# Kernel tuning notes

Hardware: AMD Instinct MI355X
Metric: run time of the kernel (lower is better)

Reference implementation:

```python
import jax, jax.numpy as jnp
import numpy as np

B, S, D, P = 8, 2048, 512, 64  # batch, seq, num_embed_hidden, num_attention_project


def setup_inputs() -> dict:
    key = jax.random.key(0)
    ks = jax.random.split(key, 9)
    sd = 1.0 / np.sqrt(D)
    sp = 1.0 / np.sqrt(P)
    return {
        "query": jax.random.normal(ks[0], (B, S, D), dtype=jnp.float32),
        "attention_mask": jnp.ones((B, S), dtype=jnp.float32),
        "Wq": jax.random.uniform(ks[1], (D, P), jnp.float32, -sd, sd),
        "bq": jax.random.uniform(ks[2], (P,), jnp.float32, -sd, sd),
        "Wk": jax.random.uniform(ks[3], (D, P), jnp.float32, -sd, sd),
        "bk": jax.random.uniform(ks[4], (P,), jnp.float32, -sd, sd),
        "Wv": jax.random.uniform(ks[5], (D, P), jnp.float32, -sd, sd),
        "bv": jax.random.uniform(ks[6], (P,), jnp.float32, -sd, sd),
        "Wo": jax.random.uniform(ks[7], (P, D), jnp.float32, -sp, sp),
        "bo": jax.random.uniform(ks[8], (D,), jnp.float32, -sp, sp),
    }


def reference(query, attention_mask, Wq, bq, Wk, bk, Wv, bv, Wo, bo):
    q = jnp.einsum("bsd,dp->bsp", query, Wq) + bq  # [B,S,P]
    k = jnp.einsum("bsd,dp->bsp", query, Wk) + bk
    v = jnp.einsum("bsd,dp->bsp", query, Wv) + bv
    scores = jnp.einsum("bsp,btp->bst", q, k) / jnp.sqrt(jnp.float32(P))  # [B,S,S]
    # Faithful to original: mask broadcast over last axis via unsqueeze(-1) -> masks rows
    scores = scores + (1.0 - attention_mask[:, :, None]) * -10000.0
    weights = jax.nn.softmax(scores, axis=-1)
    weighted = jnp.einsum("bst,btp->bsp", weights, v)
    return jnp.einsum("bsp,pd->bsd", weighted, Wo) + bo
```

## Files before the change

kernel.cpp:

```cpp
#include <hip/hip_runtime.h>
#include <hip/hip_bf16.h>
#include <math.h>

constexpr int B = 8;
constexpr int S = 2048;
constexpr int D = 512;
constexpr int P = 64;
constexpr float SCALE = 0.125f;

typedef short bf16x8 __attribute__((ext_vector_type(8)));
typedef float f32x4 __attribute__((ext_vector_type(4)));
typedef unsigned int u32;

__device__ __forceinline__ unsigned short f2bf(float x) {
  __hip_bfloat16 h = __float2bfloat16(x);
  return __builtin_bit_cast(unsigned short, h);
}
__device__ __forceinline__ float bf2f(unsigned short u) {
  unsigned int v = (unsigned int)u << 16;
  return __builtin_bit_cast(float, v);
}


__global__ __launch_bounds__(256) void prep_w(
    const float* __restrict__ Wq, const float* __restrict__ Wk,
    const float* __restrict__ Wv, const float* __restrict__ Wo,
    unsigned short* __restrict__ Bfrag, unsigned short* __restrict__ Wofrag) {
  const int i = blockIdx.x * 256 + threadIdx.x;
  if (i < 192 * 512) {
    const int d = i / 192;
    const int n = i - d * 192;
    const float* W = (n < 64) ? Wq : (n < 128) ? Wk : Wv;
    const float val = W[d * 64 + (n & 63)];
    const int nt = n >> 4, l15 = n & 15;
    const int k16 = d >> 5, l4 = (d >> 3) & 3, j = d & 7;
    Bfrag[(((nt * 16 + k16) * 4 + l4) * 16 + l15) * 8 + j] = f2bf(val);
  }
  if (i < 64 * 512) {
    const int k = i >> 9;
    const int n = i & 511;
    const float val = Wo[k * 512 + n];
    const int ct = n >> 4, l15 = n & 15;
    const int h = k >> 5, l4 = (k >> 3) & 3, j = k & 7;
    Wofrag[(((ct * 2 + h) * 4 + l4) * 16 + l15) * 8 + j] = f2bf(val);
  }
}

__global__ __launch_bounds__(256, 4) void qkv_mfma(
    const float* __restrict__ query, const unsigned short* __restrict__ Bfrag,
    const float* __restrict__ bq, const float* __restrict__ bk,
    const float* __restrict__ bv, unsigned short* __restrict__ qfrag,
    unsigned short* __restrict__ kfrag, unsigned short* __restrict__ vfrag) {
  __shared__ __align__(16) unsigned short Aq[16 * 512];

  const int tid = threadIdx.x;
  const int w = tid >> 6;
  const int l = tid & 63;
  const int l15 = l & 15;
  const int l4 = l >> 4;
  const int s0 = blockIdx.x * 16;
  const int kb0 = blockIdx.x & 15;

  const float* qsrc = query + (size_t)s0 * D;
#pragma unroll
  for (int step = 0; step < 4; ++step) {
    const int row = step * 4 + w;
    const float* pf = qsrc + row * D + l * 8;
    const float4 x = *(const float4*)pf;
    const float4 y = *(const float4*)(pf + 4);
    bf16x8 u;
    u[0] = (short)f2bf(x.x); u[1] = (short)f2bf(x.y);
    u[2] = (short)f2bf(x.z); u[3] = (short)f2bf(x.w);
    u[4] = (short)f2bf(y.x); u[5] = (short)f2bf(y.y);
    u[6] = (short)f2bf(y.z); u[7] = (short)f2bf(y.w);
    *(bf16x8*)&Aq[row * 512 + ((l ^ (row & 7)) << 3)] = u;
  }
  __syncthreads();

  f32x4 acc[3];
#pragma unroll
  for (int nt = 0; nt < 3; ++nt) acc[nt] = (f32x4){0.f, 0.f, 0.f, 0.f};

#pragma unroll
  for (int kk = 0; kk < 16; ++kk) {
    const int k16 = (kk + kb0) & 15;
    const int aslot = (k16 * 4 + l4) ^ (l15 & 7);
    const bf16x8 af = *(const bf16x8*)&Aq[l15 * 512 + (aslot << 3)];
#pragma unroll
    for (int nt = 0; nt < 3; ++nt) {
      const int ntg = w * 3 + nt;
      const bf16x8 bf =
          *(const bf16x8*)(Bfrag + ((size_t)(ntg * 16 + k16) * 64 + l) * 8);
      acc[nt] = __builtin_amdgcn_mfma_f32_16x16x32_bf16(af, bf, acc[nt], 0, 0,
                                                        0);
    }
  }

  const int b = s0 >> 11;
  const size_t bbase = (size_t)b * (S * P);
#pragma unroll
  for (int nt = 0; nt < 3; ++nt) {
    const int col = w * 48 + nt * 16 + l15;
    const int mat = col >> 6;
    const int p = col & 63;
    const float bb = ((mat == 0) ? bq : (mat == 1) ? bk : bv)[p];
#pragma unroll
    for (int r = 0; r < 4; ++r) {
      const int s = s0 + l4 * 4 + r;
      const int t = s & 2047;
      const float vl = acc[nt][r] + bb;
      if (mat == 2) {
        const int tb = t >> 5, chv = (t >> 3) & 3, jv = t & 7;
        const int pcv = p >> 4, rowv = p & 15;
        vfrag[bbase + (((size_t)(tb * 4 + pcv) * 4 + chv) * 16 + rowv) * 8 +
              jv] = f2bf(vl);
      } else {
        const int tile = t >> 4, rowin = t & 15;
        const int h = p >> 5, chp = (p >> 3) & 3, j = p & 7;
        unsigned short* dst = (mat == 0) ? qfrag : kfrag;
        dst[bbase + (((size_t)(tile * 2 + h) * 4 + chp) * 16 + rowin) * 8 +
            j] = f2bf(mat == 0 ? vl * SCALE : vl);
      }
    }
  }
}

__global__ __launch_bounds__(1024, 4) void attn_fused(
    const unsigned short* __restrict__ qfrag,
    const unsigned short* __restrict__ kfrag,
    const unsigned short* __restrict__ vfrag,
    const unsigned short* __restrict__ Wofrag, const float* __restrict__ bo,
    float* __restrict__ out) {
  __shared__ __align__(16) unsigned char smem[131072];
  __shared__ float l_s[16][32];

  const int tid = threadIdx.x;
  const int w = tid >> 6;
  const int lane = tid & 63;
  const int l15 = lane & 15;
  const int l4 = lane >> 4;
  const int qg = w & 1;
  const int th = w >> 1;

  const int blk = blockIdx.x;
  const int b = blk & 7;
  const int qt = blk >> 3;
  const int s0 = qt * 64;
  const int wst = qt & 3;

  const size_t bbase = (size_t)b * (S * P);
  const unsigned short* qf = qfrag + bbase;
  const unsigned short* kf = kfrag + bbase;
  const unsigned short* vf = vfrag + bbase;

  unsigned short* e_w = (unsigned short*)smem + w * 4096;

  bf16x8 aq[2][2];
#pragma unroll
  for (int st = 0; st < 2; ++st)
#pragma unroll
    for (int h = 0; h < 2; ++h)
      aq[st][h] =
          *(const bf16x8*)(qf +
                           ((size_t)(((s0 >> 4) + qg * 2 + st) * 2 + h) * 64 +
                            lane) *
                               8);

  f32x4 acc[2][4];
#pragma unroll
  for (int st = 0; st < 2; ++st)
#pragma unroll
    for (int pc = 0; pc < 4; ++pc) acc[st][pc] = (f32x4){0.f, 0.f, 0.f, 0.f};
  float lpart[2][4] = {{0.f, 0.f, 0.f, 0.f}, {0.f, 0.f, 0.f, 0.f}};

  for (int win = 0; win < 4; ++win) {
    const int wi = (win + wst) & 3;
    const int t0 = th * 256 + wi * 64;
    unsigned short* e_s = e_w + (win & 1) * 2048;

    bf16x8 bk[4][2];
#pragma unroll
    for (int nt = 0; nt < 4; ++nt)
#pragma unroll
      for (int h = 0; h < 2; ++h)
        bk[nt][h] =
            *(const bf16x8*)(kf +
                             ((size_t)(((t0 >> 4) + nt) * 2 + h) * 64 + lane) *
                                 8);

#pragma unroll
    for (int st = 0; st < 2; ++st) {
      f32x4 sc[4];
#pragma unroll
      for (int nt = 0; nt < 4; ++nt) {
        f32x4 c = (f32x4){0.f, 0.f, 0.f, 0.f};
        c = __builtin_amdgcn_mfma_f32_16x16x32_bf16(aq[st][0], bk[nt][0], c, 0,
                                                    0, 0);
        sc[nt] = __builtin_amdgcn_mfma_f32_16x16x32_bf16(aq[st][1], bk[nt][1],
                                                         c, 0, 0, 0);
      }
#pragma unroll
      for (int nt = 0; nt < 4; ++nt) {
        const int ch = nt * 2 + (l15 >> 3);
#pragma unroll
        for (int r = 0; r < 4; ++r) {
          const int rr = l4 * 4 + r;
          const unsigned short eu = f2bf(__expf(sc[nt][r]));
          lpart[st][r] += bf2f(eu);
          e_s[st * 1024 + rr * 64 + ((ch ^ (rr & 7)) << 3) + (l15 & 7)] = eu;
        }
      }
    }

    bf16x8 bv[4][2];
#pragma unroll
    for (int pc = 0; pc < 4; ++pc)
#pragma unroll
      for (int kk = 0; kk < 2; ++kk)
        bv[pc][kk] =
            *(const bf16x8*)(vf +
                             ((size_t)(((t0 >> 5) + kk) * 4 + pc) * 64 + lane) *
                                 8);

#pragma unroll
    for (int st = 0; st < 2; ++st) {
      bf16x8 ae[2];
#pragma unroll
      for (int kk = 0; kk < 2; ++kk)
        ae[kk] = *(const bf16x8*)&e_s[st * 1024 + l15 * 64 +
                                      (((kk * 4 + l4) ^ (l15 & 7)) << 3)];
#pragma unroll
      for (int pc = 0; pc < 4; ++pc) {
        acc[st][pc] = __builtin_amdgcn_mfma_f32_16x16x32_bf16(
            ae[0], bv[pc][0], acc[st][pc], 0, 0, 0);
        acc[st][pc] = __builtin_amdgcn_mfma_f32_16x16x32_bf16(
            ae[1], bv[pc][1], acc[st][pc], 0, 0, 0);
      }
    }
  }

#pragma unroll
  for (int st = 0; st < 2; ++st)
#pragma unroll
    for (int r = 0; r < 4; ++r) {
      float v = lpart[st][r];
      v += __shfl_xor(v, 1, 64);
      v += __shfl_xor(v, 2, 64);
      v += __shfl_xor(v, 4, 64);
      v += __shfl_xor(v, 8, 64);
      if (l15 == 0) l_s[w][st * 16 + l4 * 4 + r] = v;
    }

  __syncthreads();

  float* pacc = (float*)smem;
  if (th > 0) {
#pragma unroll
    for (int st = 0; st < 2; ++st)
#pragma unroll
      for (int pc = 0; pc < 4; ++pc)
#pragma unroll
        for (int r = 0; r < 4; ++r)
          pacc[((size_t)(qg * 7 + th - 1) * 32 + st * 16 + l4 * 4 + r) * 64 +
               pc * 16 + l15] = acc[st][pc][r];
  }
  __syncthreads();

  unsigned short* wnorm = (unsigned short*)(smem + 114688);
  if (th == 0) {
#pragma unroll
    for (int st = 0; st < 2; ++st) {
      float rl[4];
#pragma unroll
      for (int r = 0; r < 4; ++r) {
        const int row = st * 16 + l4 * 4 + r;
        float ls = 0.f;
#pragma unroll
        for (int t8 = 0; t8 < 8; ++t8) ls += l_s[t8 * 2 + qg][row];
        rl[r] = 1.f / ls;
      }
#pragma unroll
      for (int pc = 0; pc < 4; ++pc)
#pragma unroll
        for (int r = 0; r < 4; ++r) {
          float s = acc[st][pc][r];
#pragma unroll
          for (int j = 0; j < 7; ++j)
            s += pacc[((size_t)(qg * 7 + j) * 32 + st * 16 + l4 * 4 + r) * 64 +
                      pc * 16 + l15];
          wnorm[(qg * 32 + st * 16 + l4 * 4 + r) * 64 + pc * 16 + l15] =
              f2bf(s * rl[r]);
        }
    }
  }
  __syncthreads();

  const int sub = w & 3;
  const int chq = w >> 2;
  const bf16x8 a0 = *(const bf16x8*)&wnorm[(sub * 16 + l15) * 64 + l4 * 8];
  const bf16x8 a1 =
      *(const bf16x8*)&wnorm[(sub * 16 + l15) * 64 + 32 + l4 * 8];
  const size_t orow0 = (size_t)b * S + s0 + sub * 16;
#pragma unroll
  for (int ct = 0; ct < 8; ++ct) {
    const int ctg = chq * 8 + ((ct + (blk & 7)) & 7);
    const bf16x8 b0 =
        *(const bf16x8*)(Wofrag + ((size_t)(ctg * 2 + 0) * 64 + lane) * 8);
    const bf16x8 b1 =
        *(const bf16x8*)(Wofrag + ((size_t)(ctg * 2 + 1) * 64 + lane) * 8);
    f32x4 c = (f32x4){0.f, 0.f, 0.f, 0.f};
    c = __builtin_amdgcn_mfma_f32_16x16x32_bf16(a0, b0, c, 0, 0, 0);
    c = __builtin_amdgcn_mfma_f32_16x16x32_bf16(a1, b1, c, 0, 0, 0);
    const int col = ctg * 16 + l15;
    const float bb = bo[col];
#pragma unroll
    for (int r = 0; r < 4; ++r)
      out[(orow0 + l4 * 4 + r) * D + col] = c[r] + bb;
  }
}

extern "C" void kernel_launch(void* const* d_in, const int* in_sizes, int n_in,
                              void* d_out, int out_size, void* d_ws,
                              size_t ws_size, hipStream_t stream) {
  const float* query = (const float*)d_in[0];
  const float* Wq = (const float*)d_in[2];
  const float* bq = (const float*)d_in[3];
  const float* Wk = (const float*)d_in[4];
  const float* bk = (const float*)d_in[5];
  const float* Wv = (const float*)d_in[6];
  const float* bv = (const float*)d_in[7];
  const float* Wo = (const float*)d_in[8];
  const float* bo = (const float*)d_in[9];
  float* out = (float*)d_out;

  const size_t proj = (size_t)B * S * P;
  unsigned short* qfr = (unsigned short*)d_ws;
  unsigned short* kfr = qfr + proj;
  unsigned short* vfr = kfr + proj;
  unsigned short* Bfrag = vfr + proj;
  unsigned short* Wofrag = Bfrag + 192 * 512;

  prep_w<<<384, 256, 0, stream>>>(Wq, Wk, Wv, Wo, Bfrag, Wofrag);
  qkv_mfma<<<1024, 256, 0, stream>>>(query, Bfrag, bq, bk, bv, qfr, kfr, vfr);
  attn_fused<<<256, 1024, 0, stream>>>(qfr, kfr, vfr, Wofrag, bo, out);
}
```

Measured before the change: 138.4 us.

## Transpose MFMA operands for packed stores and parallelize partial-sum reduction

The QKV projection kernel swaps MFMA operand order for Q and K so each lane holds 4 consecutive projection columns. Q/K/V fragments are then written as packed 4-element stores instead of scattered 2-byte stores. The attention kernel likewise computes transposed score tiles so exp values are written to LDS as packed 8-byte chunks with a byte-level XOR swizzle. The cross-wave reduction of partial outputs now spreads over all 16 waves using vectorized float4 LDS reads, instead of 2 waves doing serial sums. This adds an extra barrier and relies on subtle fragment index remapping being correct.

```diff
diff --git a/kernel.cpp b/kernel.cpp
--- a/kernel.cpp
+++ b/kernel.cpp
@@ -9,8 +9,8 @@
 constexpr float SCALE = 0.125f;
 
 typedef short bf16x8 __attribute__((ext_vector_type(8)));
+typedef short s16x4 __attribute__((ext_vector_type(4)));
 typedef float f32x4 __attribute__((ext_vector_type(4)));
-typedef unsigned int u32;
 
 __device__ __forceinline__ unsigned short f2bf(float x) {
   __hip_bfloat16 h = __float2bfloat16(x);
@@ -79,50 +79,59 @@
 
   f32x4 acc[3];
 #pragma unroll
-  for (int nt = 0; nt < 3; ++nt) acc[nt] = (f32x4){0.f, 0.f, 0.f, 0.f};
+  for (int m = 0; m < 3; ++m) acc[m] = (f32x4){0.f, 0.f, 0.f, 0.f};
 
 #pragma unroll
   for (int kk = 0; kk < 16; ++kk) {
     const int k16 = (kk + kb0) & 15;
     const int aslot = (k16 * 4 + l4) ^ (l15 & 7);
     const bf16x8 af = *(const bf16x8*)&Aq[l15 * 512 + (aslot << 3)];
-#pragma unroll
-    for (int nt = 0; nt < 3; ++nt) {
-      const int ntg = w * 3 + nt;
-      const bf16x8 bf =
-          *(const bf16x8*)(Bfrag + ((size_t)(ntg * 16 + k16) * 64 + l) * 8);
-      acc[nt] = __builtin_amdgcn_mfma_f32_16x16x32_bf16(af, bf, acc[nt], 0, 0,
-                                                        0);
-    }
-  }
-
-  const int b = s0 >> 11;
-  const size_t bbase = (size_t)b * (S * P);
-#pragma unroll
-  for (int nt = 0; nt < 3; ++nt) {
-    const int col = w * 48 + nt * 16 + l15;
-    const int mat = col >> 6;
-    const int p = col & 63;
-    const float bb = ((mat == 0) ? bq : (mat == 1) ? bk : bv)[p];
-#pragma unroll
-    for (int r = 0; r < 4; ++r) {
-      const int s = s0 + l4 * 4 + r;
-      const int t = s & 2047;
-      const float vl = acc[nt][r] + bb;
-      if (mat == 2) {
-        const int tb = t >> 5, chv = (t >> 3) & 3, jv = t & 7;
-        const int pcv = p >> 4, rowv = p & 15;
-        vfrag[bbase + (((size_t)(tb * 4 + pcv) * 4 + chv) * 16 + rowv) * 8 +
-              jv] = f2bf(vl);
-      } else {
-        const int tile = t >> 4, rowin = t & 15;
-        const int h = p >> 5, chp = (p >> 3) & 3, j = p & 7;
-        unsigned short* dst = (mat == 0) ? qfrag : kfrag;
-        dst[bbase + (((size_t)(tile * 2 + h) * 4 + chp) * 16 + rowin) * 8 +
-            j] = f2bf(mat == 0 ? vl * SCALE : vl);
-      }
-    }
-  }
+    const bf16x8 bfq =
+        *(const bf16x8*)(Bfrag + ((size_t)(w * 16 + k16) * 64 + l) * 8);
+    const bf16x8 bfk =
+        *(const bf16x8*)(Bfrag + ((size_t)((4 + w) * 16 + k16) * 64 + l) * 8);
+    const bf16x8 bfv =
+        *(const bf16x8*)(Bfrag + ((size_t)((8 + w) * 16 + k16) * 64 + l) * 8);
+    acc[0] = __builtin_amdgcn_mfma_f32_16x16x32_bf16(bfq, af, acc[0], 0, 0, 0);
+    acc[1] = __builtin_amdgcn_mfma_f32_16x16x32_bf16(bfk, af, acc[1], 0, 0, 0);
+    acc[2] = __builtin_amdgcn_mfma_f32_16x16x32_bf16(af, bfv, acc[2], 0, 0, 0);
+  }
+
+  const int bidx = s0 >> 11;
+  const size_t bbase = (size_t)bidx * (S * P);
+  const int S0 = s0 & 2047;
+
+  const int p0 = w * 16 + l4 * 4;
+  const float4 bq4 = *(const float4*)(bq + p0);
+  const float4 bk4 = *(const float4*)(bk + p0);
+  const size_t qkoff =
+      bbase +
+      ((((size_t)(S0 >> 4) * 2 + (p0 >> 5)) * 4 + ((p0 >> 3) & 3)) * 16 +
+       l15) * 8 +
+      (p0 & 7);
+  s16x4 pq, pkk;
+  pq[0] = (short)f2bf((acc[0][0] + bq4.x) * SCALE);
+  pq[1] = (short)f2bf((acc[0][1] + bq4.y) * SCALE);
+  pq[2] = (short)f2bf((acc[0][2] + bq4.z) * SCALE);
+  pq[3] = (short)f2bf((acc[0][3] + bq4.w) * SCALE);
+  pkk[0] = (short)f2bf(acc[1][0] + bk4.x);
+  pkk[1] = (short)f2bf(acc[1][1] + bk4.y);
+  pkk[2] = (short)f2bf(acc[1][2] + bk4.z);
+  pkk[3] = (short)f2bf(acc[1][3] + bk4.w);
+  *(s16x4*)(qfrag + qkoff) = pq;
+  *(s16x4*)(kfrag + qkoff) = pkk;
+
+  const float bbv = bv[w * 16 + l15];
+  const int chv = ((S0 >> 3) + (l4 >> 1)) & 3;
+  const size_t voff =
+      bbase + ((((size_t)(S0 >> 5) * 4 + w) * 4 + chv) * 16 + l15) * 8 +
+      (l4 & 1) * 4;
+  s16x4 pv;
+  pv[0] = (short)f2bf(acc[2][0] + bbv);
+  pv[1] = (short)f2bf(acc[2][1] + bbv);
+  pv[2] = (short)f2bf(acc[2][2] + bbv);
+  pv[3] = (short)f2bf(acc[2][3] + bbv);
+  *(s16x4*)(vfrag + voff) = pv;
 }
 
 __global__ __launch_bounds__(1024, 4) void attn_fused(
@@ -153,7 +162,8 @@
   const unsigned short* kf = kfrag + bbase;
   const unsigned short* vf = vfrag + bbase;
 
-  unsigned short* e_w = (unsigned short*)smem + w * 4096;
+  unsigned char* e_w = smem + w * 8192;
+  const int xm = (l15 & 7) << 4;
 
   bf16x8 aq[2][2];
 #pragma unroll
@@ -171,12 +181,12 @@
   for (int st = 0; st < 2; ++st)
 #pragma unroll
     for (int pc = 0; pc < 4; ++pc) acc[st][pc] = (f32x4){0.f, 0.f, 0.f, 0.f};
-  float lpart[2][4] = {{0.f, 0.f, 0.f, 0.f}, {0.f, 0.f, 0.f, 0.f}};
+  float lpart[2] = {0.f, 0.f};
 
   for (int win = 0; win < 4; ++win) {
     const int wi = (win + wst) & 3;
     const int t0 = th * 256 + wi * 64;
-    unsigned short* e_s = e_w + (win & 1) * 2048;
+    unsigned char* epb = e_w + (win & 1) * 4096;
 
     bf16x8 bk[4][2];
 #pragma unroll
@@ -188,28 +198,14 @@
                              ((size_t)(((t0 >> 4) + nt) * 2 + h) * 64 + lane) *
                                  8);
 
-#pragma unroll
-    for (int st = 0; st < 2; ++st) {
-      f32x4 sc[4];
-#pragma unroll
-      for (int nt = 0; nt < 4; ++nt) {
-        f32x4 c = (f32x4){0.f, 0.f, 0.f, 0.f};
-        c = __builtin_amdgcn_mfma_f32_16x16x32_bf16(aq[st][0], bk[nt][0], c, 0,
-                                                    0, 0);
-        sc[nt] = __builtin_amdgcn_mfma_f32_16x16x32_bf16(aq[st][1], bk[nt][1],
-                                                         c, 0, 0, 0);
-      }
-#pragma unroll
-      for (int nt = 0; nt < 4; ++nt) {
-        const int ch = nt * 2 + (l15 >> 3);
-#pragma unroll
-        for (int r = 0; r < 4; ++r) {
-          const int rr = l4 * 4 + r;
-          const unsigned short eu = f2bf(__expf(sc[nt][r]));
-          lpart[st][r] += bf2f(eu);
-          e_s[st * 1024 + rr * 64 + ((ch ^ (rr & 7)) << 3) + (l15 & 7)] = eu;
-        }
-      }
+    f32x4 sc[4];
+#pragma unroll
+    for (int nt = 0; nt < 4; ++nt) {
+      f32x4 c = (f32x4){0.f, 0.f, 0.f, 0.f};
+      c = __builtin_amdgcn_mfma_f32_16x16x32_bf16(bk[nt][0], aq[0][0], c, 0,
+                                                  0, 0);
+      sc[nt] = __builtin_amdgcn_mfma_f32_16x16x32_bf16(bk[nt][1], aq[0][1], c,
+                                                       0, 0, 0);
     }
 
     bf16x8 bv[4][2];
@@ -223,12 +219,40 @@
                                  8);
 
 #pragma unroll
+    for (int nt = 0; nt < 4; ++nt) {
+      s16x4 pk;
+#pragma unroll
+      for (int r = 0; r < 4; ++r) pk[r] = (short)f2bf(__expf(sc[nt][r]));
+#pragma unroll
+      for (int r = 0; r < 4; ++r) lpart[0] += bf2f((unsigned short)pk[r]);
+      *(s16x4*)(epb + l15 * 128 + ((nt * 32 + l4 * 8) ^ xm)) = pk;
+    }
+
+#pragma unroll
+    for (int nt = 0; nt < 4; ++nt) {
+      f32x4 c = (f32x4){0.f, 0.f, 0.f, 0.f};
+      c = __builtin_amdgcn_mfma_f32_16x16x32_bf16(bk[nt][0], aq[1][0], c, 0,
+                                                  0, 0);
+      sc[nt] = __builtin_amdgcn_mfma_f32_16x16x32_bf16(bk[nt][1], aq[1][1], c,
+                                                       0, 0, 0);
+    }
+#pragma unroll
+    for (int nt = 0; nt < 4; ++nt) {
+      s16x4 pk;
+#pragma unroll
+      for (int r = 0; r < 4; ++r) pk[r] = (short)f2bf(__expf(sc[nt][r]));
+#pragma unroll
+      for (int r = 0; r < 4; ++r) lpart[1] += bf2f((unsigned short)pk[r]);
+      *(s16x4*)(epb + 2048 + l15 * 128 + ((nt * 32 + l4 * 8) ^ xm)) = pk;
+    }
+
+#pragma unroll
     for (int st = 0; st < 2; ++st) {
       bf16x8 ae[2];
 #pragma unroll
       for (int kk = 0; kk < 2; ++kk)
-        ae[kk] = *(const bf16x8*)&e_s[st * 1024 + l15 * 64 +
-                                      (((kk * 4 + l4) ^ (l15 & 7)) << 3)];
+        ae[kk] = *(const bf16x8*)(epb + st * 2048 + l15 * 128 +
+                                  ((kk * 64 + l4 * 16) ^ xm));
 #pragma unroll
       for (int pc = 0; pc < 4; ++pc) {
         acc[st][pc] = __builtin_amdgcn_mfma_f32_16x16x32_bf16(
@@ -240,59 +264,53 @@
   }
 
 #pragma unroll
+  for (int st = 0; st < 2; ++st) {
+    float v = lpart[st];
+    v += __shfl_xor(v, 16, 64);
+    v += __shfl_xor(v, 32, 64);
+    if (l4 == 0) l_s[w][st * 16 + l15] = v;
+  }
+
+  __syncthreads();
+
+  float* pacc = (float*)smem;
+#pragma unroll
   for (int st = 0; st < 2; ++st)
 #pragma unroll
-    for (int r = 0; r < 4; ++r) {
-      float v = lpart[st][r];
-      v += __shfl_xor(v, 1, 64);
-      v += __shfl_xor(v, 2, 64);
-      v += __shfl_xor(v, 4, 64);
-      v += __shfl_xor(v, 8, 64);
-      if (l15 == 0) l_s[w][st * 16 + l4 * 4 + r] = v;
-    }
-
-  __syncthreads();
-
-  float* pacc = (float*)smem;
-  if (th > 0) {
-#pragma unroll
-    for (int st = 0; st < 2; ++st)
-#pragma unroll
-      for (int pc = 0; pc < 4; ++pc)
-#pragma unroll
-        for (int r = 0; r < 4; ++r)
-          pacc[((size_t)(qg * 7 + th - 1) * 32 + st * 16 + l4 * 4 + r) * 64 +
-               pc * 16 + l15] = acc[st][pc][r];
-  }
-  __syncthreads();
-
-  unsigned short* wnorm = (unsigned short*)(smem + 114688);
-  if (th == 0) {
-#pragma unroll
-    for (int st = 0; st < 2; ++st) {
-      float rl[4];
+    for (int pc = 0; pc < 4; ++pc)
 #pragma unroll
       for (int r = 0; r < 4; ++r) {
         const int row = st * 16 + l4 * 4 + r;
-        float ls = 0.f;
-#pragma unroll
-        for (int t8 = 0; t8 < 8; ++t8) ls += l_s[t8 * 2 + qg][row];
-        rl[r] = 1.f / ls;
+        pacc[((size_t)w * 32 + row) * 64 + ((pc ^ l4) * 16) + l15] =
+            acc[st][pc][r];
       }
-#pragma unroll
-      for (int pc = 0; pc < 4; ++pc)
-#pragma unroll
-        for (int r = 0; r < 4; ++r) {
-          float s = acc[st][pc][r];
-#pragma unroll
-          for (int j = 0; j < 7; ++j)
-            s += pacc[((size_t)(qg * 7 + j) * 32 + st * 16 + l4 * 4 + r) * 64 +
-                      pc * 16 + l15];
-          wnorm[(qg * 32 + st * 16 + l4 * 4 + r) * 64 + pc * 16 + l15] =
-              f2bf(s * rl[r]);
-        }
-    }
-  }
+  __syncthreads();
+
+  const int R = w * 4 + l4;
+  const int qgR = R >> 5;
+  const int r32 = R & 31;
+  const int csw = (r32 >> 2) & 3;
+  const int coff = (((l15 >> 2) ^ csw) * 16) + (l15 & 3) * 4;
+  float4 s4 = {0.f, 0.f, 0.f, 0.f};
+#pragma unroll
+  for (int t8 = 0; t8 < 8; ++t8) {
+    const float4 p4 =
+        *(const float4*)&pacc[((size_t)(t8 * 2 + qgR) * 32 + r32) * 64 + coff];
+    s4.x += p4.x; s4.y += p4.y; s4.z += p4.z; s4.w += p4.w;
+  }
+  float ls = 0.f;
+#pragma unroll
+  for (int t8 = 0; t8 < 8; ++t8) ls += l_s[t8 * 2 + qgR][r32];
+  const float inv = 1.f / ls;
+  s16x4 wn;
+  wn[0] = (short)f2bf(s4.x * inv);
+  wn[1] = (short)f2bf(s4.y * inv);
+  wn[2] = (short)f2bf(s4.z * inv);
+  wn[3] = (short)f2bf(s4.w * inv);
+  __syncthreads();
+
+  unsigned short* wnorm = (unsigned short*)smem;
+  *(s16x4*)&wnorm[R * 64 + l15 * 4] = wn;
   __syncthreads();
 
   const int sub = w & 3;
```

Measured after the change: 156.6 us. 13.2% more time.
